# Optimization experiments

Measured on AMD Instinct MI355X. Metric: run time of the kernel, lower is better.

The kernel has to match this reference:

```python
import jax, jax.numpy as jnp
import numpy as np

B, N = 1, 384
EDGE_DIM, MID_DIM = 128, 128
C_IN, C_OUT = 32, 32
LN_EPS = 1e-5


def _layer_norm(h, g, b):
    m = jnp.mean(h, axis=-1, keepdims=True)
    v = jnp.var(h, axis=-1, keepdims=True)
    return (h - m) * jax.lax.rsqrt(v + LN_EPS) * g + b


def setup_inputs() -> dict:
    key = jax.random.key(0)
    ks = jax.random.split(key, 8)
    s_e = 1.0 / np.sqrt(EDGE_DIM)
    s_m = 1.0 / np.sqrt(MID_DIM)
    return {
        "x": jax.random.normal(ks[0], (B, N, N, C_IN, 1), jnp.float32),
        "edge_info": jax.random.normal(ks[1], (B, N, N, EDGE_DIM), jnp.float32),
        "W1": jax.random.normal(ks[2], (EDGE_DIM, MID_DIM), jnp.float32) * s_e,
        "b1": jnp.zeros((MID_DIM,), jnp.float32),
        "g1": jnp.ones((MID_DIM,), jnp.float32),
        "be1": jnp.zeros((MID_DIM,), jnp.float32),
        "W2": jax.random.normal(ks[3], (MID_DIM, MID_DIM), jnp.float32) * s_m,
        "b2": jnp.zeros((MID_DIM,), jnp.float32),
        "g2": jnp.ones((MID_DIM,), jnp.float32),
        "be2": jnp.zeros((MID_DIM,), jnp.float32),
        "W3": jax.random.normal(ks[4], (MID_DIM, C_IN * C_OUT), jnp.float32) * s_m,
        "b3": jnp.zeros((C_IN * C_OUT,), jnp.float32),
    }


def reference(x, edge_info, W1, b1, g1, be1, W2, b2, g2, be2, W3, b3):
    # Edge-conditioned kernel MLP: Linear -> LN -> GELU (x2) -> Linear
    h = edge_info @ W1 + b1
    h = jax.nn.gelu(_layer_norm(h, g1, be1), approximate=False)
    h = h @ W2 + b2
    h = jax.nn.gelu(_layer_norm(h, g2, be2), approximate=False)
    k = h @ W3 + b3                                      # (b, n, n, o*i)
    k = k.reshape(*k.shape[:-1], C_OUT, C_IN)            # (b, n, n, o, i)
    # batched per-edge GEMV: sum_i k[..., o, i] * x[..., i]
    out = jnp.einsum("...oi,...i->...o", k, x[..., 0])   # (b, n, n, o)
    return out[..., None]                                # (b, n, n, o, 1)
```

## Files before the change

### kernel.cpp

```cpp
#include <hip/hip_runtime.h>


typedef __bf16 bf16x8 __attribute__((ext_vector_type(8)));
typedef __bf16 bf16x4 __attribute__((ext_vector_type(4)));
typedef float f32x4 __attribute__((ext_vector_type(4)));

#define N_EDGES 147456
#define TM 128
#define NTHR 512

__device__ __forceinline__ unsigned short f2bf(float f) {
    unsigned u = __float_as_uint(f);
    u = u + 0x7FFFu + ((u >> 16) & 1u);
    return (unsigned short)(u >> 16);
}
__device__ __forceinline__ float gelu_t(float x) {
    float z = 0.7978845608f * (x + 0.044715f * x * x * x);
    return x / (1.0f + __expf(-2.0f * z));
}
__device__ __forceinline__ void gl_lds16(const unsigned short* g, unsigned char* l) {
    __builtin_amdgcn_global_load_lds(
        (const __attribute__((address_space(1))) unsigned int*)g,
        (__attribute__((address_space(3))) unsigned int*)l, 16, 0, 0);
}

__global__ void prep_weights(const float* __restrict__ W1,
                             const float* __restrict__ W2,
                             const float* __restrict__ W3,
                             unsigned short* __restrict__ ws) {
    int t = blockIdx.x * 256 + threadIdx.x;
    if (t < 16384) {
        int k = t >> 7, n = t & 127;
        ws[n * 128 + (((k >> 3) ^ (n & 7)) << 3) + (k & 7)] = f2bf(W1[t]);
    } else if (t < 32768) {
        int j = t - 16384;
        int k = j >> 7, n = j & 127;
        ws[16384 + n * 128 + (((k >> 3) ^ (n & 7)) << 3) + (k & 7)] = f2bf(W2[j]);
    } else {
        int j = t - 32768;
        int k = j >> 10, n = j & 1023;
        int tile = n >> 7, nl = n & 127;
        ws[32768 + tile * 16384 + nl * 128 + (((k >> 3) ^ (nl & 7)) << 3) + (k & 7)]
            = f2bf(W3[j]);
    }
}

__global__ __launch_bounds__(NTHR, 4)
void fused_edge_mlp(const float* __restrict__ edge, const float* __restrict__ x,
                    const float* __restrict__ b1, const float* __restrict__ g1,
                    const float* __restrict__ be1,
                    const float* __restrict__ b2, const float* __restrict__ g2,
                    const float* __restrict__ be2,
                    const float* __restrict__ b3,
                    const unsigned short* __restrict__ wsW,
                    float* __restrict__ out) {
    __shared__ __align__(16) unsigned char sA[TM * 256];
    __shared__ __align__(16) unsigned char sW[128 * 256];

    const int t    = threadIdx.x;
    const int lane = t & 63;
    const int w    = t >> 6;
    const int e0   = blockIdx.x * TM;
    const int erow = w * 16;
    const int mrow = lane & 15;
    const int hi   = lane >> 4;
    const int swzl = (mrow & 7) << 4;

    auto stageW = [&](const unsigned short* srcW, unsigned char* dst) {
#pragma unroll
        for (int i = 0; i < 4; i++) {
            int base = w * 256 + i * 64;
            gl_lds16(srcW + (size_t)(base + lane) * 8, dst + (size_t)base * 16);
        }
    };

    auto runMM = [&](f32x4 (&acc)[8]) {
#pragma unroll
        for (int kk = 0; kk < 4; kk++) {
            int kb = (kk * 64 + hi * 16) ^ swzl;
            bf16x8 bB = *(const bf16x8*)(sA + (erow + mrow) * 256 + kb);
#pragma unroll
            for (int fn = 0; fn < 8; fn++) {
                bf16x8 a = *(const bf16x8*)(sW + (fn * 16 + mrow) * 256 + kb);
                acc[fn] = __builtin_amdgcn_mfma_f32_16x16x32_bf16(a, bB, acc[fn], 0, 0, 0);
            }
        }
    };

    auto runMM3 = [&](f32x4 (&acc)[8], const bf16x8 (&bc)[4],
                      const unsigned char* wbuf) {
#pragma unroll
        for (int kk = 0; kk < 4; kk++) {
            int kb = (kk * 64 + hi * 16) ^ swzl;
#pragma unroll
            for (int fn = 0; fn < 8; fn++) {
                bf16x8 a = *(const bf16x8*)(wbuf + (fn * 16 + mrow) * 256 + kb);
                acc[fn] = __builtin_amdgcn_mfma_f32_16x16x32_bf16(a, bc[kk], acc[fn], 0, 0, 0);
            }
        }
    };

    f32x4 xq[2];

    auto lnGelu = [&](f32x4 (&acc)[8], const float* bb, const float* gg,
                      const float* ee) {
        float hv[8][4];
        float s = 0.f, s2 = 0.f;
#pragma unroll
        for (int fn = 0; fn < 8; fn++) {
            f32x4 b4 = *(const f32x4*)(bb + fn * 16 + hi * 4);
#pragma unroll
            for (int rr = 0; rr < 4; rr++) {
                float v = acc[fn][rr] + b4[rr];
                hv[fn][rr] = v; s += v; s2 += v * v;
            }
        }
        s  += __shfl_xor(s, 16);  s  += __shfl_xor(s, 32);
        s2 += __shfl_xor(s2, 16); s2 += __shfl_xor(s2, 32);
        float mean = s * (1.0f / 128.0f);
        float rsv  = rsqrtf(s2 * (1.0f / 128.0f) - mean * mean + 1e-5f);
        int row = erow + mrow;
#pragma unroll
        for (int fn = 0; fn < 8; fn++) {
            f32x4 g4 = *(const f32x4*)(gg + fn * 16 + hi * 4);
            f32x4 e4 = *(const f32x4*)(ee + fn * 16 + hi * 4);
            bf16x4 u;
#pragma unroll
            for (int rr = 0; rr < 4; rr++) {
                float f = (hv[fn][rr] - mean) * rsv * g4[rr] + e4[rr];
                u[rr] = (__bf16)gelu_t(f);
            }
            *(bf16x4*)(sA + row * 256 + ((fn * 32 + hi * 8) ^ swzl)) = u;
        }
    };

    f32x4 voutA, voutB;
    auto gemv = [&](f32x4 (&acc)[8], int c) {
        f32x4 b3q[8];
#pragma unroll
        for (int fn = 0; fn < 8; fn++)
            b3q[fn] = *(const f32x4*)(b3 + c * 128 + fn * 16 + hi * 4);
        f32x4 pv;
#pragma unroll
        for (int o = 0; o < 4; o++) {
            float p = 0.f;
#pragma unroll
            for (int rr = 0; rr < 4; rr++) {
                p += (acc[2*o][rr]   + b3q[2*o][rr])   * xq[0][rr];
                p += (acc[2*o+1][rr] + b3q[2*o+1][rr]) * xq[1][rr];
            }
            p += __shfl_xor(p, 16);
            p += __shfl_xor(p, 32);
            pv[o] = p;
        }
        if (hi == (c >> 1)) {
            if (c & 1) voutB = pv; else voutA = pv;
        }
    };

    stageW(wsW, sW);
#pragma unroll
    for (int i = 0; i < 4; i++) {
        int c = lane + i * 64;
        int r = erow + (c >> 4), kg = c & 15;
        const float* src = edge + (size_t)(e0 + r) * 128 + kg * 8;
        float4 v0 = *(const float4*)src, v1 = *(const float4*)(src + 4);
        bf16x8 u;
        u[0] = (__bf16)v0.x; u[1] = (__bf16)v0.y; u[2] = (__bf16)v0.z; u[3] = (__bf16)v0.w;
        u[4] = (__bf16)v1.x; u[5] = (__bf16)v1.y; u[6] = (__bf16)v1.z; u[7] = (__bf16)v1.w;
        *(bf16x8*)(sA + r * 256 + ((kg * 16) ^ ((r & 7) << 4))) = u;
    }
#pragma unroll
    for (int b = 0; b < 2; b++)
        xq[b] = *(const f32x4*)(
            x + (size_t)(e0 + erow + mrow) * 32 + b * 16 + hi * 4);
    __syncthreads();

    f32x4 acc[8];
    const f32x4 zz = {0.f, 0.f, 0.f, 0.f};

#pragma unroll
    for (int j = 0; j < 8; j++) acc[j] = zz;
    runMM(acc);
    __syncthreads();
    stageW(wsW + 16384, sW);
    lnGelu(acc, b1, g1, be1);
    __syncthreads();

#pragma unroll
    for (int j = 0; j < 8; j++) acc[j] = zz;
    runMM(acc);
    __syncthreads();
    stageW(wsW + 32768, sW);
    lnGelu(acc, b2, g2, be2);
    __syncthreads();

    bf16x8 bc[4];
#pragma unroll
    for (int kk = 0; kk < 4; kk++) {
        int kb = (kk * 64 + hi * 16) ^ swzl;
        bc[kk] = *(const bf16x8*)(sA + (erow + mrow) * 256 + kb);
    }
    __syncthreads();
    stageW(wsW + 32768 + 16384, sA);

#pragma unroll
    for (int c = 0; c < 8; c++) {
#pragma unroll
        for (int j = 0; j < 8; j++) acc[j] = zz;
        runMM3(acc, bc, (c & 1) ? sA : sW);
        gemv(acc, c);
        if (c < 7) {
            __syncthreads();
            if (c < 6)
                stageW(wsW + 32768 + (size_t)(c + 2) * 16384,
                       (c & 1) ? sA : sW);
        }
    }

    {
        size_t e = (size_t)(e0 + erow + mrow);
        *(f32x4*)(out + e * 32 + hi * 8)     = voutA;
        *(f32x4*)(out + e * 32 + hi * 8 + 4) = voutB;
    }
}

extern "C" void kernel_launch(void* const* d_in, const int* in_sizes, int n_in,
                              void* d_out, int out_size, void* d_ws, size_t ws_size,
                              hipStream_t stream) {
    const float* x    = (const float*)d_in[0];
    const float* edge = (const float*)d_in[1];
    const float* W1   = (const float*)d_in[2];
    const float* b1   = (const float*)d_in[3];
    const float* g1   = (const float*)d_in[4];
    const float* be1  = (const float*)d_in[5];
    const float* W2   = (const float*)d_in[6];
    const float* b2   = (const float*)d_in[7];
    const float* g2   = (const float*)d_in[8];
    const float* be2  = (const float*)d_in[9];
    const float* W3   = (const float*)d_in[10];
    const float* b3   = (const float*)d_in[11];
    unsigned short* wsW = (unsigned short*)d_ws;
    float* outp = (float*)d_out;

    prep_weights<<<640, 256, 0, stream>>>(W1, W2, W3, wsW);
    fused_edge_mlp<<<N_EDGES / TM, NTHR, 0, stream>>>(
        edge, x, b1, g1, be1, b2, g2, be2, b3, wsW, outp);
}
```

Before: 107.8 us.

## Switch to 32x32x16 MFMA with 4 waves of 32 edges each

Replaces the 16x16x32 bf16 MFMA tiling with 32x32x16 tiles, so each of 4 waves (256 threads) handles 32 edges instead of 8 waves handling 16. The LN/GELU and GEMV epilogues are remapped to the new accumulator layout, which cuts the cross-lane shuffles to a single xor. The b3 bias term is folded out of the per-chunk GEMV into a precomputed b3·x dot product. This lowers LDS weight reads per MFMA and shuffle overhead, at the cost of more accumulator registers per wave and a lower occupancy bound.

```diff
diff --git a/kernel.cpp b/kernel.cpp
--- a/kernel.cpp
+++ b/kernel.cpp
@@ -4,10 +4,11 @@
 typedef __bf16 bf16x8 __attribute__((ext_vector_type(8)));
 typedef __bf16 bf16x4 __attribute__((ext_vector_type(4)));
 typedef float f32x4 __attribute__((ext_vector_type(4)));
+typedef float f32x16 __attribute__((ext_vector_type(16)));
 
 #define N_EDGES 147456
 #define TM 128
-#define NTHR 512
+#define NTHR 256
 
 __device__ __forceinline__ unsigned short f2bf(float f) {
     unsigned u = __float_as_uint(f);
@@ -45,7 +46,7 @@
     }
 }
 
-__global__ __launch_bounds__(NTHR, 4)
+__global__ __launch_bounds__(NTHR, 2)
 void fused_edge_mlp(const float* __restrict__ edge, const float* __restrict__ x,
                     const float* __restrict__ b1, const float* __restrict__ g1,
                     const float* __restrict__ be1,
@@ -57,112 +58,111 @@
     __shared__ __align__(16) unsigned char sA[TM * 256];
     __shared__ __align__(16) unsigned char sW[128 * 256];
 
-    const int t    = threadIdx.x;
-    const int lane = t & 63;
-    const int w    = t >> 6;
-    const int e0   = blockIdx.x * TM;
-    const int erow = w * 16;
-    const int mrow = lane & 15;
-    const int hi   = lane >> 4;
-    const int swzl = (mrow & 7) << 4;
+    const int t     = threadIdx.x;
+    const int lane  = t & 63;
+    const int w     = t >> 6;
+    const int e0    = blockIdx.x * TM;
+    const int ebase = w * 32;
+    const int r31   = lane & 31;
+    const int l5    = lane >> 5;
+    const int eloc  = ebase + r31;
+    const int swzl  = (lane & 7) << 4;
+    const f32x16 zz = {0.f,0.f,0.f,0.f,0.f,0.f,0.f,0.f,
+                       0.f,0.f,0.f,0.f,0.f,0.f,0.f,0.f};
 
     auto stageW = [&](const unsigned short* srcW, unsigned char* dst) {
 #pragma unroll
-        for (int i = 0; i < 4; i++) {
-            int base = w * 256 + i * 64;
+        for (int i = 0; i < 8; i++) {
+            int base = w * 512 + i * 64;
             gl_lds16(srcW + (size_t)(base + lane) * 8, dst + (size_t)base * 16);
         }
     };
 
-    auto runMM = [&](f32x4 (&acc)[8]) {
-#pragma unroll
-        for (int kk = 0; kk < 4; kk++) {
-            int kb = (kk * 64 + hi * 16) ^ swzl;
-            bf16x8 bB = *(const bf16x8*)(sA + (erow + mrow) * 256 + kb);
-#pragma unroll
-            for (int fn = 0; fn < 8; fn++) {
-                bf16x8 a = *(const bf16x8*)(sW + (fn * 16 + mrow) * 256 + kb);
-                acc[fn] = __builtin_amdgcn_mfma_f32_16x16x32_bf16(a, bB, acc[fn], 0, 0, 0);
-            }
-        }
-    };
-
-    auto runMM3 = [&](f32x4 (&acc)[8], const bf16x8 (&bc)[4],
+    auto runMM = [&](f32x16 (&acc)[4]) {
+#pragma unroll
+        for (int ks = 0; ks < 8; ks++) {
+            int kb = (ks * 32 + l5 * 16) ^ swzl;
+            bf16x8 b = *(const bf16x8*)(sA + eloc * 256 + kb);
+#pragma unroll
+            for (int f = 0; f < 4; f++) {
+                bf16x8 a = *(const bf16x8*)(sW + (f * 32 + r31) * 256 + kb);
+                acc[f] = __builtin_amdgcn_mfma_f32_32x32x16_bf16(
+                    a, b, (ks == 0) ? zz : acc[f], 0, 0, 0);
+            }
+        }
+    };
+
+    auto runMM3 = [&](f32x16 (&acc)[4], const bf16x8 (&bc)[8],
                       const unsigned char* wbuf) {
 #pragma unroll
-        for (int kk = 0; kk < 4; kk++) {
-            int kb = (kk * 64 + hi * 16) ^ swzl;
-#pragma unroll
-            for (int fn = 0; fn < 8; fn++) {
-                bf16x8 a = *(const bf16x8*)(wbuf + (fn * 16 + mrow) * 256 + kb);
-                acc[fn] = __builtin_amdgcn_mfma_f32_16x16x32_bf16(a, bc[kk], acc[fn], 0, 0, 0);
-            }
-        }
-    };
-
-    f32x4 xq[2];
-
-    auto lnGelu = [&](f32x4 (&acc)[8], const float* bb, const float* gg,
+        for (int ks = 0; ks < 8; ks++) {
+            int kb = (ks * 32 + l5 * 16) ^ swzl;
+#pragma unroll
+            for (int f = 0; f < 4; f++) {
+                bf16x8 a = *(const bf16x8*)(wbuf + (f * 32 + r31) * 256 + kb);
+                acc[f] = __builtin_amdgcn_mfma_f32_32x32x16_bf16(
+                    a, bc[ks], (ks == 0) ? zz : acc[f], 0, 0, 0);
+            }
+        }
+    };
+
+    auto lnGelu = [&](f32x16 (&acc)[4], const float* bb, const float* gg,
                       const float* ee) {
-        float hv[8][4];
         float s = 0.f, s2 = 0.f;
 #pragma unroll
-        for (int fn = 0; fn < 8; fn++) {
-            f32x4 b4 = *(const f32x4*)(bb + fn * 16 + hi * 4);
-#pragma unroll
-            for (int rr = 0; rr < 4; rr++) {
-                float v = acc[fn][rr] + b4[rr];
-                hv[fn][rr] = v; s += v; s2 += v * v;
-            }
-        }
-        s  += __shfl_xor(s, 16);  s  += __shfl_xor(s, 32);
-        s2 += __shfl_xor(s2, 16); s2 += __shfl_xor(s2, 32);
+        for (int f = 0; f < 4; f++)
+#pragma unroll
+            for (int q = 0; q < 4; q++) {
+                f32x4 b4 = *(const f32x4*)(bb + f * 32 + q * 8 + l5 * 4);
+#pragma unroll
+                for (int j = 0; j < 4; j++) {
+                    float v = acc[f][q * 4 + j] + b4[j];
+                    s += v; s2 += v * v;
+                }
+            }
+        s  += __shfl_xor(s, 32);
+        s2 += __shfl_xor(s2, 32);
         float mean = s * (1.0f / 128.0f);
         float rsv  = rsqrtf(s2 * (1.0f / 128.0f) - mean * mean + 1e-5f);
-        int row = erow + mrow;
-#pragma unroll
-        for (int fn = 0; fn < 8; fn++) {
-            f32x4 g4 = *(const f32x4*)(gg + fn * 16 + hi * 4);
-            f32x4 e4 = *(const f32x4*)(ee + fn * 16 + hi * 4);
-            bf16x4 u;
-#pragma unroll
-            for (int rr = 0; rr < 4; rr++) {
-                float f = (hv[fn][rr] - mean) * rsv * g4[rr] + e4[rr];
-                u[rr] = (__bf16)gelu_t(f);
-            }
-            *(bf16x4*)(sA + row * 256 + ((fn * 32 + hi * 8) ^ swzl)) = u;
-        }
-    };
-
-    f32x4 voutA, voutB;
-    auto gemv = [&](f32x4 (&acc)[8], int c) {
-        f32x4 b3q[8];
-#pragma unroll
-        for (int fn = 0; fn < 8; fn++)
-            b3q[fn] = *(const f32x4*)(b3 + c * 128 + fn * 16 + hi * 4);
-        f32x4 pv;
-#pragma unroll
-        for (int o = 0; o < 4; o++) {
+#pragma unroll
+        for (int f = 0; f < 4; f++)
+#pragma unroll
+            for (int q = 0; q < 4; q++) {
+                f32x4 b4 = *(const f32x4*)(bb + f * 32 + q * 8 + l5 * 4);
+                f32x4 g4 = *(const f32x4*)(gg + f * 32 + q * 8 + l5 * 4);
+                f32x4 e4 = *(const f32x4*)(ee + f * 32 + q * 8 + l5 * 4);
+                bf16x4 u;
+#pragma unroll
+                for (int j = 0; j < 4; j++) {
+                    float v = acc[f][q * 4 + j] + b4[j];
+                    float fv = (v - mean) * rsv * g4[j] + e4[j];
+                    u[j] = (__bf16)gelu_t(fv);
+                }
+                *(bf16x4*)(sA + eloc * 256 + ((f * 64 + q * 16 + l5 * 8) ^ swzl)) = u;
+            }
+    };
+
+    f32x4 xv[4];
+    f32x4 vout4[4];
+    auto gemv = [&](f32x16 (&acc)[4], int c) {
+#pragma unroll
+        for (int f = 0; f < 4; f++) {
             float p = 0.f;
 #pragma unroll
-            for (int rr = 0; rr < 4; rr++) {
-                p += (acc[2*o][rr]   + b3q[2*o][rr])   * xq[0][rr];
-                p += (acc[2*o+1][rr] + b3q[2*o+1][rr]) * xq[1][rr];
-            }
-            p += __shfl_xor(p, 16);
+            for (int q = 0; q < 4; q++)
+#pragma unroll
+                for (int j = 0; j < 4; j++)
+                    p += acc[f][q * 4 + j] * xv[q][j];
             p += __shfl_xor(p, 32);
-            pv[o] = p;
-        }
-        if (hi == (c >> 1)) {
-            if (c & 1) voutB = pv; else voutA = pv;
+            if ((c >> 2) == l5) vout4[c & 3][f] += p;
         }
     };
 
     stageW(wsW, sW);
 #pragma unroll
-    for (int i = 0; i < 4; i++) {
+    for (int i = 0; i < 8; i++) {
         int c = lane + i * 64;
-        int r = erow + (c >> 4), kg = c & 15;
+        int r = ebase + (c >> 4), kg = c & 15;
         const float* src = edge + (size_t)(e0 + r) * 128 + kg * 8;
         float4 v0 = *(const float4*)src, v1 = *(const float4*)(src + 4);
         bf16x8 u;
@@ -171,43 +171,48 @@
         *(bf16x8*)(sA + r * 256 + ((kg * 16) ^ ((r & 7) << 4))) = u;
     }
 #pragma unroll
-    for (int b = 0; b < 2; b++)
-        xq[b] = *(const f32x4*)(
-            x + (size_t)(e0 + erow + mrow) * 32 + b * 16 + hi * 4);
-    __syncthreads();
-
-    f32x4 acc[8];
-    const f32x4 zz = {0.f, 0.f, 0.f, 0.f};
-
-#pragma unroll
-    for (int j = 0; j < 8; j++) acc[j] = zz;
+    for (int q = 0; q < 4; q++)
+        xv[q] = *(const f32x4*)(
+            x + (size_t)(e0 + eloc) * 32 + q * 8 + l5 * 4);
+    __syncthreads();
+
+    f32x16 acc[4];
+
     runMM(acc);
     __syncthreads();
     stageW(wsW + 16384, sW);
     lnGelu(acc, b1, g1, be1);
     __syncthreads();
 
-#pragma unroll
-    for (int j = 0; j < 8; j++) acc[j] = zz;
     runMM(acc);
     __syncthreads();
     stageW(wsW + 32768, sW);
     lnGelu(acc, b2, g2, be2);
     __syncthreads();
 
-    bf16x8 bc[4];
-#pragma unroll
-    for (int kk = 0; kk < 4; kk++) {
-        int kb = (kk * 64 + hi * 16) ^ swzl;
-        bc[kk] = *(const bf16x8*)(sA + (erow + mrow) * 256 + kb);
-    }
+    bf16x8 bc[8];
+#pragma unroll
+    for (int ks = 0; ks < 8; ks++)
+        bc[ks] = *(const bf16x8*)(sA + eloc * 256 + ((ks * 32 + l5 * 16) ^ swzl));
+#pragma unroll
+    for (int c = 0; c < 8; c++)
+#pragma unroll
+        for (int f = 0; f < 4; f++) {
+            float p = 0.f;
+#pragma unroll
+            for (int q = 0; q < 4; q++) {
+                f32x4 b4 = *(const f32x4*)(b3 + c * 128 + f * 32 + q * 8 + l5 * 4);
+#pragma unroll
+                for (int j = 0; j < 4; j++) p += b4[j] * xv[q][j];
+            }
+            p += __shfl_xor(p, 32);
+            if ((c >> 2) == l5) vout4[c & 3][f] = p;
+        }
     __syncthreads();
     stageW(wsW + 32768 + 16384, sA);
 
 #pragma unroll
     for (int c = 0; c < 8; c++) {
-#pragma unroll
-        for (int j = 0; j < 8; j++) acc[j] = zz;
         runMM3(acc, bc, (c & 1) ? sA : sW);
         gemv(acc, c);
         if (c < 7) {
@@ -219,9 +224,10 @@
     }
 
     {
-        size_t e = (size_t)(e0 + erow + mrow);
-        *(f32x4*)(out + e * 32 + hi * 8)     = voutA;
-        *(f32x4*)(out + e * 32 + hi * 8 + 4) = voutB;
+        size_t e = (size_t)(e0 + eloc);
+#pragma unroll
+        for (int cb = 0; cb < 4; cb++)
+            *(f32x4*)(out + e * 32 + l5 * 16 + cb * 4) = vout4[cb];
     }
 }
 
```

Result: slower. 144.1 us (+33.6%).
